# Performance work log

Hardware: AMD Instinct MI355X
Metric: run time of the kernel (lower is better)

## Reference

```python
import jax, jax.numpy as jnp
import numpy as np

D_MODEL = 1024
NUM_HEAD = 16
D_K = D_MODEL // NUM_HEAD


def setup_inputs() -> dict:
    key = jax.random.key(0)
    ks = jax.random.split(key, 9)
    s = 1.0 / np.sqrt(D_MODEL)
    x = jax.random.normal(ks[0], (2, 2048, D_MODEL), dtype=jnp.float32)
    Wq = jax.random.uniform(ks[1], (D_MODEL, D_MODEL), jnp.float32, -s, s)
    bq = jax.random.uniform(ks[2], (D_MODEL,), jnp.float32, -s, s)
    Wk = jax.random.uniform(ks[3], (D_MODEL, D_MODEL), jnp.float32, -s, s)
    bk = jax.random.uniform(ks[4], (D_MODEL,), jnp.float32, -s, s)
    Wv = jax.random.uniform(ks[5], (D_MODEL, D_MODEL), jnp.float32, -s, s)
    bv = jax.random.uniform(ks[6], (D_MODEL,), jnp.float32, -s, s)
    Wo = jax.random.uniform(ks[7], (D_MODEL, D_MODEL), jnp.float32, -s, s)
    bo = jax.random.uniform(ks[8], (D_MODEL,), jnp.float32, -s, s)
    return {"x": x, "Wq": Wq, "bq": bq, "Wk": Wk, "bk": bk,
            "Wv": Wv, "bv": bv, "Wo": Wo, "bo": bo}


def reference(x, Wq, bq, Wk, bk, Wv, bv, Wo, bo):
    b, n, d = x.shape
    h, dk = NUM_HEAD, D_K
    # Linear projections (torch Linear: x @ W.T + b)
    q = (x @ Wq.T + bq).reshape(b, n, h, dk).transpose(0, 2, 1, 3)  # [b,h,n,dk]
    k = (x @ Wk.T + bk).reshape(b, n, h, dk).transpose(0, 2, 1, 3)
    v = (x @ Wv.T + bv).reshape(b, n, h, dk).transpose(0, 2, 1, 3)
    scores = jnp.einsum('bhqd,bhkd->bhqk', q, k) / jnp.sqrt(jnp.float32(dk))
    attn = jax.nn.softmax(scores, axis=-1)  # [b,h,n,n]
    out = jnp.einsum('bhqk,bhkd->bhqd', attn, v)
    out = out.transpose(0, 2, 1, 3).reshape(b, n, d)
    return out @ Wo.T + bo
```

## Files before the change

kernel.cpp:

```cpp
#include <hip/hip_runtime.h>

#define BATCH   2
#define SEQ     2048
#define DMODEL  1024
#define NHEAD   16
#define DKH     64
#define MTOT    (BATCH*SEQ)
#define KDIM    DMODEL

#define XB    0u
#define WQB   (4u*1024u*1024u)
#define WKB   (5u*1024u*1024u)
#define WVB   (6u*1024u*1024u)
#define WOB   (7u*1024u*1024u)
#define QOFF  (8u*1024u*1024u)
#define KOFF  (12u*1024u*1024u)
#define VOFF  (16u*1024u*1024u)
#define OOFF  (20u*1024u*1024u)

typedef __bf16 bf16x8 __attribute__((ext_vector_type(8)));
typedef __bf16 bf16x4 __attribute__((ext_vector_type(4)));
typedef float  f32x4  __attribute__((ext_vector_type(4)));
typedef float  f32x16 __attribute__((ext_vector_type(16)));

__device__ __forceinline__ void async16(const __bf16* g, __bf16* l) {
  __builtin_amdgcn_global_load_lds(
      (const __attribute__((address_space(1))) void*)g,
      (__attribute__((address_space(3))) void*)l, 16, 0, 0);
}

__device__ __forceinline__ unsigned cvtpk_bf16(float lo, float hi) {
  unsigned r;
  asm("v_cvt_pk_bf16_f32 %0, %1, %2" : "=v"(r) : "v"(lo), "v"(hi));
  return r;
}
__device__ __forceinline__ void plswap(unsigned& a, unsigned& b) {
  asm("v_permlane32_swap_b32 %0, %1" : "+v"(a), "+v"(b));
}

__global__ __launch_bounds__(256) void cvt_fp32_bf16(
    const float* __restrict__ x,  const float* __restrict__ wq,
    const float* __restrict__ wk, const float* __restrict__ wv,
    const float* __restrict__ wo, __bf16* __restrict__ ws)
{
  const float* src; __bf16* dst; int n;
  switch (blockIdx.y) {
    case 0:  src = x;  dst = ws + XB;  n = 4 * 1024 * 1024; break;
    case 1:  src = wq; dst = ws + WQB; n = 1024 * 1024;     break;
    case 2:  src = wk; dst = ws + WKB; n = 1024 * 1024;     break;
    case 3:  src = wv; dst = ws + WVB; n = 1024 * 1024;     break;
    default: src = wo; dst = ws + WOB; n = 1024 * 1024;     break;
  }
  const int i = (blockIdx.x * 256 + threadIdx.x) * 8;
  if (i < n) {
    const float4 a = *(const float4*)(src + i);
    const float4 b = *(const float4*)(src + i + 4);
    bf16x8 o;
    o[0] = (__bf16)a.x; o[1] = (__bf16)a.y; o[2] = (__bf16)a.z; o[3] = (__bf16)a.w;
    o[4] = (__bf16)b.x; o[5] = (__bf16)b.y; o[6] = (__bf16)b.z; o[7] = (__bf16)b.w;
    *(bf16x8*)(dst + i) = o;
  }
}

__device__ __forceinline__ void gemm128_core(
    const __bf16* __restrict__ A, const __bf16* __restrict__ W,
    int m0, int n0, __bf16* lds, f32x4 (&acc)[4][4])
{
  __bf16* A_lds = lds;
  __bf16* B_lds = lds + 4096;
  const int t    = threadIdx.x;
  const int w    = t >> 6;
  const int lane = t & 63;
  const int ln15 = lane & 15;
  const int quad = lane >> 4;
  const int wr   = (w >> 1) << 6;
  const int wc   = (w & 1) << 6;

#pragma unroll
  for (int i = 0; i < 4; ++i)
#pragma unroll
    for (int j = 0; j < 4; ++j) acc[i][j] = (f32x4){0.f, 0.f, 0.f, 0.f};

  for (int kt = 0; kt < KDIM; kt += 32) {
    __syncthreads();
#pragma unroll
    for (int issue = 0; issue < 2; ++issue) {
      const int cbase = issue * 256 + (w << 6);
      const int c     = cbase + lane;
      const int row   = c >> 2;
      const int goff  = ((c & 3) ^ (row & 3)) << 3;
      async16(A + (size_t)(m0 + row) * KDIM + kt + goff, A_lds + cbase * 8);
      async16(W + (size_t)(n0 + row) * KDIM + kt + goff, B_lds + cbase * 8);
    }
    __syncthreads();

    bf16x8 af[4], bfr[4];
#pragma unroll
    for (int i = 0; i < 4; ++i) {
      const int row = wr + i * 16 + ln15;
      af[i] = *(const bf16x8*)&A_lds[row * 32 + ((quad ^ (row & 3)) << 3)];
    }
#pragma unroll
    for (int j = 0; j < 4; ++j) {
      const int row = wc + j * 16 + ln15;
      bfr[j] = *(const bf16x8*)&B_lds[row * 32 + ((quad ^ (row & 3)) << 3)];
    }
#pragma unroll
    for (int i = 0; i < 4; ++i)
#pragma unroll
      for (int j = 0; j < 4; ++j)
        acc[i][j] = __builtin_amdgcn_mfma_f32_16x16x32_bf16(af[i], bfr[j], acc[i][j], 0, 0, 0);
  }
}

__global__ __launch_bounds__(256) void qkv_gemm(
    const __bf16* __restrict__ X,
    const __bf16* __restrict__ Wq, const float* __restrict__ bq,
    const __bf16* __restrict__ Wk, const float* __restrict__ bk,
    const __bf16* __restrict__ Wv, const float* __restrict__ bv,
    __bf16* __restrict__ ws)
{
  __shared__ __align__(16) __bf16 lds[128 * 64];

  const int z = blockIdx.z;
  const __bf16* W    = (z == 0) ? Wq : (z == 1) ? Wk : Wv;
  const float*  bias = (z == 0) ? bq : (z == 1) ? bk : bv;
  __bf16* out = ws + ((z == 0) ? QOFF : (z == 1) ? KOFF : VOFF);
  const float scale = (z == 0) ? 0.125f * 1.44269504088896f : 1.0f;

  const int m0 = blockIdx.x * 128;
  const int n0 = blockIdx.y * 128;

  f32x4 acc[4][4];
  gemm128_core(X, W, m0, n0, lds, acc);

  const int t = threadIdx.x, w = t >> 6, lane = t & 63;
  const int ln15 = lane & 15, quad = lane >> 4;
  const int wr = (w >> 1) << 6, wc = (w & 1) << 6;

  float bj4[4];
#pragma unroll
  for (int j = 0; j < 4; ++j) bj4[j] = bias[n0 + wc + j * 16 + ln15];

  __syncthreads();
  __bf16* scr = lds + (w << 10);

  const int bb = m0 >> 11;
  const int s_base = (m0 & 2047) + wr;
  const int h = (n0 + wc) >> 6;

  if (z != 2) {
    const int rdrow = lane & 15, rdseg = lane >> 4;
#pragma unroll
    for (int i = 0; i < 4; ++i) {
#pragma unroll
      for (int j = 0; j < 4; ++j)
#pragma unroll
        for (int rr = 0; rr < 4; ++rr)
          scr[(quad * 4 + rr) * 64 + j * 16 + ln15] =
              (__bf16)((acc[i][j][rr] + bj4[j]) * scale);
      bf16x8 v0 = *(const bf16x8*)&scr[rdrow * 64 + rdseg * 16];
      bf16x8 v1 = *(const bf16x8*)&scr[rdrow * 64 + rdseg * 16 + 8];
      const int s = s_base + i * 16 + rdrow;
      __bf16* p = out + (((size_t)(bb * NHEAD + h)) * SEQ + s) * DKH + rdseg * 16;
      *(bf16x8*)p = v0;
      *(bf16x8*)&p[8] = v1;
    }
  } else {
#pragma unroll
    for (int i = 0; i < 4; ++i) {
#pragma unroll
      for (int j = 0; j < 4; ++j) {
        bf16x4 pk;
#pragma unroll
        for (int rr = 0; rr < 4; ++rr) pk[rr] = (__bf16)(acc[i][j][rr] + bj4[j]);
        *(bf16x4*)&scr[(j * 16 + ln15) * 16 + quad * 4] = pk;
      }
      bf16x8 c0 = *(const bf16x8*)&scr[lane * 16];
      bf16x8 c1 = *(const bf16x8*)&scr[lane * 16 + 8];
      __bf16* p = out + (((size_t)(bb * NHEAD + h)) * DKH + lane) * SEQ
                      + s_base + i * 16;
      *(bf16x8*)p = c0;
      *(bf16x8*)&p[8] = c1;
    }
  }
}

__global__ __launch_bounds__(256) void out_gemm(
    const __bf16* __restrict__ A, const __bf16* __restrict__ Wo,
    const float* __restrict__ bo, float* __restrict__ out)
{
  __shared__ __align__(16) __bf16 lds[6144];
  __bf16* A_lds = lds;
  __bf16* B_lds = lds + 2048;

  const int m0 = blockIdx.x * 64;
  const int n0 = blockIdx.y * 128;

  const int t = threadIdx.x, w = t >> 6, lane = t & 63;
  const int ln15 = lane & 15, quad = lane >> 4;

  f32x4 acc[4][2];
#pragma unroll
  for (int i = 0; i < 4; ++i)
#pragma unroll
    for (int j = 0; j < 2; ++j) acc[i][j] = (f32x4){0.f, 0.f, 0.f, 0.f};

  for (int kt = 0; kt < KDIM; kt += 32) {
    __syncthreads();
    {
      const int c = (w << 6) + lane;
      const int row = c >> 2;
      const int goff = ((c & 3) ^ (row & 3)) << 3;
      async16(A + (size_t)(m0 + row) * KDIM + kt + goff, A_lds + c * 8);
    }
#pragma unroll
    for (int issue = 0; issue < 2; ++issue) {
      const int cbase = issue * 256 + (w << 6);
      const int c = cbase + lane;
      const int row = c >> 2;
      const int goff = ((c & 3) ^ (row & 3)) << 3;
      async16(Wo + (size_t)(n0 + row) * KDIM + kt + goff, B_lds + cbase * 8);
    }
    __syncthreads();

    bf16x8 af[4], bfr[2];
#pragma unroll
    for (int i = 0; i < 4; ++i) {
      const int row = i * 16 + ln15;
      af[i] = *(const bf16x8*)&A_lds[row * 32 + ((quad ^ (row & 3)) << 3)];
    }
#pragma unroll
    for (int j = 0; j < 2; ++j) {
      const int row = (w << 5) + j * 16 + ln15;
      bfr[j] = *(const bf16x8*)&B_lds[row * 32 + ((quad ^ (row & 3)) << 3)];
    }
#pragma unroll
    for (int i = 0; i < 4; ++i)
#pragma unroll
      for (int j = 0; j < 2; ++j)
        acc[i][j] = __builtin_amdgcn_mfma_f32_16x16x32_bf16(af[i], bfr[j], acc[i][j], 0, 0, 0);
  }

  float bj2[2];
#pragma unroll
  for (int j = 0; j < 2; ++j) bj2[j] = bo[n0 + (w << 5) + j * 16 + ln15];

  __syncthreads();
  float* scrf = (float*)lds + (w << 9);

  const int rdrow = lane & 15, rdseg = lane >> 4;
#pragma unroll
  for (int i = 0; i < 4; ++i) {
#pragma unroll
    for (int j = 0; j < 2; ++j) {
      f32x4 v;
#pragma unroll
      for (int rr = 0; rr < 4; ++rr) v[rr] = acc[i][j][rr] + bj2[j];
      *(f32x4*)&scrf[(j * 16 + ln15) * 16 + quad * 4] = v;
    }
    const int m = m0 + i * 16 + rdrow;
    float* p = out + (size_t)m * DMODEL + n0 + (w << 5) + rdseg * 8;
#pragma unroll
    for (int cc = 0; cc < 2; ++cc) {
      f32x4 v;
#pragma unroll
      for (int e = 0; e < 4; ++e)
        v[e] = scrf[(rdseg * 8 + cc * 4 + e) * 16 + rdrow];
      *(f32x4*)&p[cc * 4] = v;
    }
  }
}

__device__ __forceinline__ void softmax_frag(const f32x16& s, float& l,
                                             bf16x8& pfa, bf16x8& pfb)
{
  float p[16];
#pragma unroll
  for (int r = 0; r < 16; ++r) {
    p[r] = __builtin_amdgcn_exp2f(s[r]);
    l += p[r];
  }
  unsigned A0 = cvtpk_bf16(p[0],  p[1]);
  unsigned A1 = cvtpk_bf16(p[2],  p[3]);
  unsigned B0 = cvtpk_bf16(p[4],  p[5]);
  unsigned B1 = cvtpk_bf16(p[6],  p[7]);
  unsigned C0 = cvtpk_bf16(p[8],  p[9]);
  unsigned C1 = cvtpk_bf16(p[10], p[11]);
  unsigned D0 = cvtpk_bf16(p[12], p[13]);
  unsigned D1 = cvtpk_bf16(p[14], p[15]);
  plswap(A0, B0);
  plswap(A1, B1);
  plswap(C0, D0);
  plswap(C1, D1);
  union { unsigned u[4]; bf16x8 v; } ua, ub;
  ua.u[0] = A0; ua.u[1] = A1; ua.u[2] = B0; ua.u[3] = B1;
  ub.u[0] = C0; ub.u[1] = C1; ub.u[2] = D0; ub.u[3] = D1;
  pfa = ua.v;
  pfb = ub.v;
}

__device__ __forceinline__ void pvstep(const __bf16* Vs, int kh, int KS, int hl,
                                       int ln31, const bf16x8& PF,
                                       f32x16& o0, f32x16& o1)
{
  const int vchunk = (kh << 3) + 2 * KS + hl;
  bf16x8 vf0 = *(const bf16x8*)&Vs[ln31 * 128 + ((vchunk ^ (ln31 & 15)) << 3)];
  bf16x8 vf1 = *(const bf16x8*)&Vs[(32 + ln31) * 128 +
                                   ((vchunk ^ ((32 + ln31) & 15)) << 3)];
  o0 = __builtin_amdgcn_mfma_f32_32x32x16_bf16(PF, vf0, o0, 0, 0, 0);
  o1 = __builtin_amdgcn_mfma_f32_32x32x16_bf16(PF, vf1, o1, 0, 0, 0);
}

__device__ __forceinline__ void attn_tile_compute(
    const __bf16* Ks, const __bf16* Vs, const bf16x8 (&qf)[4],
    int kh, int ln31, int hl, float& l_lane, f32x16& o0, f32x16& o1)
{
#pragma unroll
  for (int half = 0; half < 2; ++half) {
    f32x16 s;
#pragma unroll
    for (int r = 0; r < 16; ++r) s[r] = 0.f;
    const int kr = (kh << 6) + half * 32 + ln31;
    __builtin_amdgcn_s_setprio(1);
#pragma unroll
    for (int ks = 0; ks < 4; ++ks) {
      bf16x8 kf = *(const bf16x8*)&Ks[kr * 64 + (((2 * ks + hl) ^ (kr & 7)) << 3)];
      s = __builtin_amdgcn_mfma_f32_32x32x16_bf16(kf, qf[ks], s, 0, 0, 0);
    }
    __builtin_amdgcn_s_setprio(0);
    bf16x8 pa, pb;
    softmax_frag(s, l_lane, pa, pb);
    __builtin_amdgcn_s_setprio(1);
    pvstep(Vs, kh, half * 2 + 0, hl, ln31, pa, o0, o1);
    pvstep(Vs, kh, half * 2 + 1, hl, ln31, pb, o0, o1);
    __builtin_amdgcn_s_setprio(0);
  }
}

__global__ __launch_bounds__(512, 2) void attn_kernel(
    const __bf16* __restrict__ Qb, const __bf16* __restrict__ Kb,
    const __bf16* __restrict__ Vtb, __bf16* __restrict__ Ob)
{
  __shared__ __align__(16) __bf16 smem[3 * 128 * 64];
  __bf16* QP = smem;
  __bf16* Ks = smem + 8192;
  __bf16* Vs = smem + 16384;

  const int t = threadIdx.x, w = t >> 6, lane = t & 63;
  const int ln31 = lane & 31, hl = lane >> 5;
  const int g  = w & 3;
  const int kh = w >> 2;
  const int bh = blockIdx.x;
  const int q0 = blockIdx.y * 128;
  const int bb = bh >> 4, hh = bh & 15;

  const __bf16* Qg = Qb + (size_t)bh * SEQ * DKH + (size_t)q0 * DKH;
  const __bf16* Kg = Kb + (size_t)bh * SEQ * DKH;
  const __bf16* Vg = Vtb + (size_t)bh * DKH * SEQ;

#pragma unroll
  for (int issue = 0; issue < 2; ++issue) {
    const int cbase = issue * 512 + (w << 6);
    const int c = cbase + lane;
    const int row = c >> 3;
    const int goff = ((c & 7) ^ (row & 7)) << 3;
    async16(Qg + (size_t)row * DKH + goff, QP + cbase * 8);
  }

  const int c0 = t, c1 = t + 512;
  const int krow0 = c0 >> 3; const int kgo0 = ((c0 & 7) ^ (krow0 & 7)) << 3;
  const int krow1 = c1 >> 3; const int kgo1 = ((c1 & 7) ^ (krow1 & 7)) << 3;
  const int vrow0 = c0 >> 4; const int vgo0 = ((c0 & 15) ^ (vrow0 & 15)) << 3;
  const int vrow1 = c1 >> 4; const int vgo1 = ((c1 & 15) ^ (vrow1 & 15)) << 3;
  const __bf16* kp0 = Kg + (size_t)krow0 * DKH + kgo0;
  const __bf16* kp1 = Kg + (size_t)krow1 * DKH + kgo1;
  const __bf16* vp0 = Vg + (size_t)vrow0 * SEQ + vgo0;
  const __bf16* vp1 = Vg + (size_t)vrow1 * SEQ + vgo1;
  __bf16* kd0 = Ks + c0 * 8;  __bf16* kd1 = Ks + c1 * 8;
  __bf16* vd0 = Vs + c0 * 8;  __bf16* vd1 = Vs + c1 * 8;

  bf16x8 krg0 = *(const bf16x8*)kp0;
  bf16x8 krg1 = *(const bf16x8*)kp1;
  bf16x8 vrg0 = *(const bf16x8*)vp0;
  bf16x8 vrg1 = *(const bf16x8*)vp1;

  __syncthreads();

  const int qrow = (g << 5) + ln31;
  bf16x8 qf[4];
#pragma unroll
  for (int ks = 0; ks < 4; ++ks) {
    const int chunk = ((2 * ks + hl) ^ (qrow & 7));
    qf[ks] = *(const bf16x8*)&QP[qrow * 64 + (chunk << 3)];
  }

  float l_lane = 0.f;
  f32x16 o0, o1;
#pragma unroll
  for (int r = 0; r < 16; ++r) { o0[r] = 0.f; o1[r] = 0.f; }

  for (int kt = 0; kt < SEQ; kt += 128) {
    __syncthreads();
    *(bf16x8*)kd0 = krg0;  *(bf16x8*)kd1 = krg1;
    *(bf16x8*)vd0 = vrg0;  *(bf16x8*)vd1 = vrg1;
    __syncthreads();
    if (kt + 128 < SEQ) {
      krg0 = *(const bf16x8*)(kp0 + (size_t)(kt + 128) * DKH);
      krg1 = *(const bf16x8*)(kp1 + (size_t)(kt + 128) * DKH);
      vrg0 = *(const bf16x8*)(vp0 + kt + 128);
      vrg1 = *(const bf16x8*)(vp1 + kt + 128);
    }
    attn_tile_compute(Ks, Vs, qf, kh, ln31, hl, l_lane, o0, o1);
  }

  __syncthreads();
  float* cmb = (float*)smem;
  const int dsw = ln31 & 7;
  l_lane += __shfl_xor(l_lane, 32);

  if (w >= 4) {
    float* base = cmb + (g << 11);
#pragma unroll
    for (int gg = 0; gg < 4; ++gg) {
      const int qq = ((2 * gg + hl) ^ dsw) << 2;
      f32x4 va, vb;
#pragma unroll
      for (int rr = 0; rr < 4; ++rr) { va[rr] = o0[4 * gg + rr]; vb[rr] = o1[4 * gg + rr]; }
      *(f32x4*)&base[ln31 * 32 + qq]        = va;
      *(f32x4*)&base[(32 + ln31) * 32 + qq] = vb;
    }
    if (hl == 0) cmb[8192 + (g << 5) + ln31] = l_lane;
  }
  __syncthreads();
  if (w < 4) {
    float* base = cmb + (g << 11);
#pragma unroll
    for (int gg = 0; gg < 4; ++gg) {
      const int qq = ((2 * gg + hl) ^ dsw) << 2;
      const f32x4 va = *(const f32x4*)&base[ln31 * 32 + qq];
      const f32x4 vb = *(const f32x4*)&base[(32 + ln31) * 32 + qq];
#pragma unroll
      for (int rr = 0; rr < 4; ++rr) { o0[4 * gg + rr] += va[rr]; o1[4 * gg + rr] += vb[rr]; }
    }
    const float inv = 1.0f / (l_lane + cmb[8192 + (g << 5) + ln31]);

#pragma unroll
    for (int r = 0; r < 16; ++r) {
      const int qi = (r & 3) + 8 * (r >> 2) + 4 * hl;
      const float iq = __shfl(inv, qi);
      const int q = q0 + (g << 5) + qi;
      __bf16* rowp = Ob + ((size_t)(bb * SEQ + q)) * DMODEL + hh * DKH;
      rowp[ln31]      = (__bf16)(o0[r] * iq);
      rowp[32 + ln31] = (__bf16)(o1[r] * iq);
    }
  }
}

extern "C" void kernel_launch(void* const* d_in, const int* in_sizes, int n_in,
                              void* d_out, int out_size, void* d_ws, size_t ws_size,
                              hipStream_t stream)
{
  const float* x  = (const float*)d_in[0];
  const float* Wq = (const float*)d_in[1];
  const float* bq = (const float*)d_in[2];
  const float* Wk = (const float*)d_in[3];
  const float* bk = (const float*)d_in[4];
  const float* Wv = (const float*)d_in[5];
  const float* bv = (const float*)d_in[6];
  const float* Wo = (const float*)d_in[7];
  const float* bo = (const float*)d_in[8];
  float*  out = (float*)d_out;
  __bf16* ws  = (__bf16*)d_ws;

  cvt_fp32_bf16<<<dim3(2048, 5, 1), 256, 0, stream>>>(x, Wq, Wk, Wv, Wo, ws);

  qkv_gemm<<<dim3(MTOT / 128, DMODEL / 128, 3), 256, 0, stream>>>(
      ws + XB, ws + WQB, bq, ws + WKB, bk, ws + WVB, bv, ws);

  attn_kernel<<<dim3(BATCH * NHEAD, SEQ / 128), 512, 0, stream>>>(
      ws + QOFF, ws + KOFF, ws + VOFF, ws + OOFF);

  out_gemm<<<dim3(MTOT / 64, DMODEL / 128), 256, 0, stream>>>(
      ws + OOFF, ws + WOB, bo, out);
}
```

Measured before the change: 187.1 us.

## Triple-buffer LDS in projection GEMMs with async prefetch two stages ahead

```diff
diff --git a/kernel.cpp b/kernel.cpp
--- a/kernel.cpp
+++ b/kernel.cpp
@@ -29,6 +29,8 @@
       (__attribute__((address_space(3))) void*)l, 16, 0, 0);
 }
 
+#define VWAIT(N) asm volatile("s_waitcnt vmcnt(" #N ")" ::: "memory")
+
 __device__ __forceinline__ unsigned cvtpk_bf16(float lo, float hi) {
   unsigned r;
   asm("v_cvt_pk_bf16_f32 %0, %1, %2" : "=v"(r) : "v"(lo), "v"(hi));
@@ -62,12 +64,48 @@
   }
 }
 
+__device__ __forceinline__ void gemm_stage128(
+    const __bf16* __restrict__ A, const __bf16* __restrict__ W,
+    int m0, int n0, int kt, __bf16* slot, int w, int lane)
+{
+#pragma unroll
+  for (int issue = 0; issue < 2; ++issue) {
+    const int cbase = issue * 256 + (w << 6);
+    const int c     = cbase + lane;
+    const int row   = c >> 2;
+    const int goff  = ((c & 3) ^ (row & 3)) << 3;
+    async16(A + (size_t)(m0 + row) * KDIM + kt + goff, slot + cbase * 8);
+    async16(W + (size_t)(n0 + row) * KDIM + kt + goff, slot + 4096 + cbase * 8);
+  }
+}
+
+__device__ __forceinline__ void gemm_step128(
+    const __bf16* slot, int wr, int wc, int ln15, int quad, f32x4 (&acc)[4][4])
+{
+  const __bf16* A_lds = slot;
+  const __bf16* B_lds = slot + 4096;
+  bf16x8 af[4], bfr[4];
+#pragma unroll
+  for (int i = 0; i < 4; ++i) {
+    const int row = wr + i * 16 + ln15;
+    af[i] = *(const bf16x8*)&A_lds[row * 32 + ((quad ^ (row & 3)) << 3)];
+  }
+#pragma unroll
+  for (int j = 0; j < 4; ++j) {
+    const int row = wc + j * 16 + ln15;
+    bfr[j] = *(const bf16x8*)&B_lds[row * 32 + ((quad ^ (row & 3)) << 3)];
+  }
+#pragma unroll
+  for (int i = 0; i < 4; ++i)
+#pragma unroll
+    for (int j = 0; j < 4; ++j)
+      acc[i][j] = __builtin_amdgcn_mfma_f32_16x16x32_bf16(af[i], bfr[j], acc[i][j], 0, 0, 0);
+}
+
 __device__ __forceinline__ void gemm128_core(
     const __bf16* __restrict__ A, const __bf16* __restrict__ W,
     int m0, int n0, __bf16* lds, f32x4 (&acc)[4][4])
 {
-  __bf16* A_lds = lds;
-  __bf16* B_lds = lds + 4096;
   const int t    = threadIdx.x;
   const int w    = t >> 6;
   const int lane = t & 63;
@@ -81,36 +119,33 @@
 #pragma unroll
     for (int j = 0; j < 4; ++j) acc[i][j] = (f32x4){0.f, 0.f, 0.f, 0.f};
 
-  for (int kt = 0; kt < KDIM; kt += 32) {
-    __syncthreads();
-#pragma unroll
-    for (int issue = 0; issue < 2; ++issue) {
-      const int cbase = issue * 256 + (w << 6);
-      const int c     = cbase + lane;
-      const int row   = c >> 2;
-      const int goff  = ((c & 3) ^ (row & 3)) << 3;
-      async16(A + (size_t)(m0 + row) * KDIM + kt + goff, A_lds + cbase * 8);
-      async16(W + (size_t)(n0 + row) * KDIM + kt + goff, B_lds + cbase * 8);
-    }
-    __syncthreads();
-
-    bf16x8 af[4], bfr[4];
-#pragma unroll
-    for (int i = 0; i < 4; ++i) {
-      const int row = wr + i * 16 + ln15;
-      af[i] = *(const bf16x8*)&A_lds[row * 32 + ((quad ^ (row & 3)) << 3)];
-    }
-#pragma unroll
-    for (int j = 0; j < 4; ++j) {
-      const int row = wc + j * 16 + ln15;
-      bfr[j] = *(const bf16x8*)&B_lds[row * 32 + ((quad ^ (row & 3)) << 3)];
-    }
-#pragma unroll
-    for (int i = 0; i < 4; ++i)
-#pragma unroll
-      for (int j = 0; j < 4; ++j)
-        acc[i][j] = __builtin_amdgcn_mfma_f32_16x16x32_bf16(af[i], bfr[j], acc[i][j], 0, 0, 0);
-  }
+  __bf16* s0 = lds;
+  __bf16* s1 = lds + 8192;
+  __bf16* s2 = lds + 16384;
+
+  gemm_stage128(A, W, m0, n0, 0,  s0, w, lane);
+  gemm_stage128(A, W, m0, n0, 32, s1, w, lane);
+
+  int kt = 0;
+#pragma unroll 1
+  for (int i3 = 0; i3 < 10; ++i3) {
+    VWAIT(4); __builtin_amdgcn_s_barrier();
+    gemm_stage128(A, W, m0, n0, kt + 64, s2, w, lane);
+    gemm_step128(s0, wr, wc, ln15, quad, acc);
+
+    VWAIT(4); __builtin_amdgcn_s_barrier();
+    gemm_stage128(A, W, m0, n0, kt + 96, s0, w, lane);
+    gemm_step128(s1, wr, wc, ln15, quad, acc);
+
+    VWAIT(4); __builtin_amdgcn_s_barrier();
+    gemm_stage128(A, W, m0, n0, kt + 128, s1, w, lane);
+    gemm_step128(s2, wr, wc, ln15, quad, acc);
+    kt += 96;
+  }
+  VWAIT(4); __builtin_amdgcn_s_barrier();
+  gemm_step128(s0, wr, wc, ln15, quad, acc);
+  VWAIT(0); __builtin_amdgcn_s_barrier();
+  gemm_step128(s1, wr, wc, ln15, quad, acc);
 }
 
 __global__ __launch_bounds__(256) void qkv_gemm(
@@ -120,7 +155,7 @@
     const __bf16* __restrict__ Wv, const float* __restrict__ bv,
     __bf16* __restrict__ ws)
 {
-  __shared__ __align__(16) __bf16 lds[128 * 64];
+  __shared__ __align__(16) __bf16 lds[24576];
 
   const int z = blockIdx.z;
   const __bf16* W    = (z == 0) ? Wq : (z == 1) ? Wk : Wv;
@@ -186,13 +221,54 @@
   }
 }
 
+__device__ __forceinline__ void out_stage(
+    const __bf16* __restrict__ A, const __bf16* __restrict__ Wo,
+    int m0, int n0, int kt, __bf16* slot, int w, int lane)
+{
+  {
+    const int c = (w << 6) + lane;
+    const int row = c >> 2;
+    const int goff = ((c & 3) ^ (row & 3)) << 3;
+    async16(A + (size_t)(m0 + row) * KDIM + kt + goff, slot + c * 8);
+  }
+#pragma unroll
+  for (int issue = 0; issue < 2; ++issue) {
+    const int cbase = issue * 256 + (w << 6);
+    const int c = cbase + lane;
+    const int row = c >> 2;
+    const int goff = ((c & 3) ^ (row & 3)) << 3;
+    async16(Wo + (size_t)(n0 + row) * KDIM + kt + goff, slot + 2048 + cbase * 8);
+  }
+}
+
+__device__ __forceinline__ void out_step(
+    const __bf16* slot, int w, int ln15, int quad, f32x4 (&acc)[4][2])
+{
+  const __bf16* A_lds = slot;
+  const __bf16* B_lds = slot + 2048;
+  bf16x8 af[4], bfr[2];
+#pragma unroll
+  for (int i = 0; i < 4; ++i) {
+    const int row = i * 16 + ln15;
+    af[i] = *(const bf16x8*)&A_lds[row * 32 + ((quad ^ (row & 3)) << 3)];
+  }
+#pragma unroll
+  for (int j = 0; j < 2; ++j) {
+    const int row = (w << 5) + j * 16 + ln15;
+    bfr[j] = *(const bf16x8*)&B_lds[row * 32 + ((quad ^ (row & 3)) << 3)];
+  }
+#pragma unroll
+  for (int i = 0; i < 4; ++i)
+#pragma unroll
+    for (int j = 0; j < 2; ++j)
+      acc[i][j] = __builtin_amdgcn_mfma_f32_16x16x32_bf16(af[i], bfr[j], acc[i][j], 0, 0, 0);
+}
+
 __global__ __launch_bounds__(256) void out_gemm(
     const __bf16* __restrict__ A, const __bf16* __restrict__ Wo,
     const float* __restrict__ bo, float* __restrict__ out)
 {
-  __shared__ __align__(16) __bf16 lds[6144];
-  __bf16* A_lds = lds;
-  __bf16* B_lds = lds + 2048;
+  __shared__ __align__(16) __bf16 lds[18432];
 
   const int m0 = blockIdx.x * 64;
   const int n0 = blockIdx.y * 128;
@@ -206,41 +282,33 @@
 #pragma unroll
     for (int j = 0; j < 2; ++j) acc[i][j] = (f32x4){0.f, 0.f, 0.f, 0.f};
 
-  for (int kt = 0; kt < KDIM; kt += 32) {
-    __syncthreads();
-    {
-      const int c = (w << 6) + lane;
-      const int row = c >> 2;
-      const int goff = ((c & 3) ^ (row & 3)) << 3;
-      async16(A + (size_t)(m0 + row) * KDIM + kt + goff, A_lds + c * 8);
-    }
-#pragma unroll
-    for (int issue = 0; issue < 2; ++issue) {
-      const int cbase = issue * 256 + (w << 6);
-      const int c = cbase + lane;
-      const int row = c >> 2;
-      const int goff = ((c & 3) ^ (row & 3)) << 3;
-      async16(Wo + (size_t)(n0 + row) * KDIM + kt + goff, B_lds + cbase * 8);
-    }
-    __syncthreads();
-
-    bf16x8 af[4], bfr[2];
-#pragma unroll
-    for (int i = 0; i < 4; ++i) {
-      const int row = i * 16 + ln15;
-      af[i] = *(const bf16x8*)&A_lds[row * 32 + ((quad ^ (row & 3)) << 3)];
-    }
-#pragma unroll
-    for (int j = 0; j < 2; ++j) {
-      const int row = (w << 5) + j * 16 + ln15;
-      bfr[j] = *(const bf16x8*)&B_lds[row * 32 + ((quad ^ (row & 3)) << 3)];
-    }
-#pragma unroll
-    for (int i = 0; i < 4; ++i)
-#pragma unroll
-      for (int j = 0; j < 2; ++j)
-        acc[i][j] = __builtin_amdgcn_mfma_f32_16x16x32_bf16(af[i], bfr[j], acc[i][j], 0, 0, 0);
-  }
+  __bf16* s0 = lds;
+  __bf16* s1 = lds + 6144;
+  __bf16* s2 = lds + 12288;
+
+  out_stage(A, Wo, m0, n0, 0,  s0, w, lane);
+  out_stage(A, Wo, m0, n0, 32, s1, w, lane);
+
+  int kt = 0;
+#pragma unroll 1
+  for (int i3 = 0; i3 < 10; ++i3) {
+    VWAIT(3); __builtin_amdgcn_s_barrier();
+    out_stage(A, Wo, m0, n0, kt + 64, s2, w, lane);
+    out_step(s0, w, ln15, quad, acc);
+
+    VWAIT(3); __builtin_amdgcn_s_barrier();
+    out_stage(A, Wo, m0, n0, kt + 96, s0, w, lane);
+    out_step(s1, w, ln15, quad, acc);
+
+    VWAIT(3); __builtin_amdgcn_s_barrier();
+    out_stage(A, Wo, m0, n0, kt + 128, s1, w, lane);
+    out_step(s2, w, ln15, quad, acc);
+    kt += 96;
+  }
+  VWAIT(3); __builtin_amdgcn_s_barrier();
+  out_step(s0, w, ln15, quad, acc);
+  VWAIT(0); __builtin_amdgcn_s_barrier();
+  out_step(s1, w, ln15, quad, acc);
 
   float bj2[2];
 #pragma unroll
```

Measured after the change: 182.5 us. 1.03x faster.
